# Kernel optimization log

Measured on AMD Instinct MI355X. Metric: run time of the kernel, lower is better.

The kernel has to match this reference:

```python
import jax, jax.numpy as jnp
import numpy as np

D_MODEL = 1024
NUM_HEADS = 16
HEAD_DIM = D_MODEL // NUM_HEADS


def setup_inputs() -> dict:
    key = jax.random.key(0)
    k_x, k_wqkv, k_bqkv, k_wo, k_bo = jax.random.split(key, 5)
    x = jax.random.normal(k_x, (2, 2048, D_MODEL), dtype=jnp.float32)
    s = 1.0 / np.sqrt(D_MODEL)
    W_qkv = jax.random.uniform(k_wqkv, (D_MODEL, 3 * D_MODEL), jnp.float32, -s, s)
    b_qkv = jax.random.uniform(k_bqkv, (3 * D_MODEL,), jnp.float32, -s, s)
    W_o = jax.random.uniform(k_wo, (D_MODEL, D_MODEL), jnp.float32, -s, s)
    b_o = jax.random.uniform(k_bo, (D_MODEL,), jnp.float32, -s, s)
    return {"x": x, "W_qkv": W_qkv, "b_qkv": b_qkv, "W_o": W_o, "b_o": b_o}


def reference(x, W_qkv, b_qkv, W_o, b_o):
    B, S, D = x.shape
    # fused QKV projection: [B,S,3D]
    qkv = jnp.einsum('bsd,de->bse', x, W_qkv) + b_qkv
    # [B,S,H,3*hd] -> [B,H,S,3*hd]
    qkv = qkv.reshape(B, S, NUM_HEADS, 3 * HEAD_DIM).transpose(0, 2, 1, 3)
    q, k, v = jnp.split(qkv, 3, axis=-1)  # each [B,H,S,hd]
    scale = 1.0 / jnp.sqrt(jnp.asarray(HEAD_DIM, dtype=x.dtype))
    scores = jnp.einsum('bhqd,bhkd->bhqk', q, k) * scale  # [B,H,S,S]
    attn = jax.nn.softmax(scores, axis=-1)
    values = jnp.einsum('bhqk,bhkd->bhqd', attn, v)  # [B,H,S,hd]
    values = values.transpose(0, 2, 1, 3).reshape(B, S, D)
    out = jnp.einsum('bsd,de->bse', values, W_o) + b_o
    return out
```

## Files before the change

### kernel.cpp

```cpp
#include <hip/hip_runtime.h>
#include <stdint.h>
#include <stddef.h>

typedef _Float16 f16;
typedef _Float16 f16x8 __attribute__((ext_vector_type(8)));
typedef _Float16 f16x4 __attribute__((ext_vector_type(4)));
typedef float    f32x2 __attribute__((ext_vector_type(2)));
typedef float    f32x4 __attribute__((ext_vector_type(4)));
typedef float    f32x16 __attribute__((ext_vector_type(16)));
typedef int      i32x4 __attribute__((ext_vector_type(4)));
typedef int      i32x2 __attribute__((ext_vector_type(2)));

#define S_LEN 2048
#define DM    1024
#define NH    16
#define HD    64
#define NTOK  4096
#define NQKV  3072
#define QSCALE 0.18033688011112042f

#if __has_builtin(__builtin_amdgcn_exp2f)
#define EXP2(x) __builtin_amdgcn_exp2f(x)
#else
#define EXP2(x) __expf((x) * 0.69314718055994531f)
#endif

__device__ __forceinline__ void gl_lds16(const void* g, void* l) {
  __builtin_amdgcn_global_load_lds(
      (const __attribute__((address_space(1))) void*)g,
      (__attribute__((address_space(3))) void*)l, 16, 0, 0);
}

__device__ __forceinline__ void pl32_swap(int& a, int& b) {
#if __has_builtin(__builtin_amdgcn_permlane32_swap)
  i32x2 r = __builtin_amdgcn_permlane32_swap(a, b, false, false);
  a = r.x; b = r.y;
#else
  asm volatile("v_permlane32_swap_b32 %0, %1" : "+v"(a), "+v"(b));
#endif
}

__device__ __forceinline__ float swap_half(float x, int hi) {
  int a = __builtin_bit_cast(int, x);
  int b = a;
  pl32_swap(a, b);
  return __builtin_bit_cast(float, hi ? a : b);
}

__device__ __forceinline__ int pkrtz(float a, float b) {
  auto h = __builtin_amdgcn_cvt_pkrtz(a, b);
  return __builtin_bit_cast(int, h);
}

__device__ __forceinline__ f16x8 mk_frag(int a, int b, int c, int d) {
  i32x4 v = {a, b, c, d};
  return __builtin_bit_cast(f16x8, v);
}

__device__ __forceinline__ f32x2 pk2(const f32x16& v, int i) {
  f32x2 r = {v[2*i], v[2*i+1]};
  return r;
}

__global__ __launch_bounds__(256) void cvt_f16_kernel(const float* __restrict__ in,
                                                      f16* __restrict__ out, int n) {
  int i = (blockIdx.x * 256 + threadIdx.x) * 8;
  if (i >= n) return;
  float4 a = *(const float4*)(in + i);
  float4 b = *(const float4*)(in + i + 4);
  f16x8 v = {(f16)a.x,(f16)a.y,(f16)a.z,(f16)a.w,(f16)b.x,(f16)b.y,(f16)b.z,(f16)b.w};
  *(f16x8*)(out + i) = v;
}

__global__ __launch_bounds__(256) void cvt_tr_kernel(const float* __restrict__ in,
                                                     f16* __restrict__ out, int R, int C) {
  __shared__ float t[32][33];
  int c0 = blockIdx.x * 32, r0 = blockIdx.y * 32;
  int tx = threadIdx.x, ty = threadIdx.y;
  #pragma unroll
  for (int i = 0; i < 4; ++i)
    t[ty + i*8][tx] = in[(size_t)(r0 + ty + i*8) * C + c0 + tx];
  __syncthreads();
  #pragma unroll
  for (int i = 0; i < 4; ++i)
    out[(size_t)(c0 + ty + i*8) * R + r0 + tx] = (f16)t[tx][ty + i*8];
}

template<int EPI>
__global__ __launch_bounds__(256) void gemm128_kernel(
    const f16* __restrict__ A, const f16* __restrict__ Bt,
    const float* __restrict__ bias,
    f16* __restrict__ qb, f16* __restrict__ kb, f16* __restrict__ vtb,
    float* __restrict__ out)
{
  __shared__ f16 As[128*32];
  __shared__ f16 Bs[128*32];
  const int tid = threadIdx.x;
  const int wid = tid >> 6, lane = tid & 63;
  const int g = lane >> 4, r = lane & 15;
  const int m0 = blockIdx.x * 128, n0 = blockIdx.y * 128;
  const int wm = (wid >> 1) * 64, wn = (wid & 1) * 64;

  f32x4 acc[4][4] = {};
  const int srow = tid >> 2;
  const int sch  = tid & 3;

  for (int kt = 0; kt < DM/32; ++kt) {
    const int k0 = kt * 32;
    __syncthreads();
    #pragma unroll
    for (int c = 0; c < 2; ++c) {
      int row = c*64 + srow;
      int sw = (sch ^ ((row >> 1) & 3)) * 8;
      gl_lds16(A  + (size_t)(m0 + row) * DM + k0 + sw, (char*)As + c*4096 + tid*16);
      gl_lds16(Bt + (size_t)(n0 + row) * DM + k0 + sw, (char*)Bs + c*4096 + tid*16);
    }
    __syncthreads();
    f16x8 a[4], b[4];
    #pragma unroll
    for (int mt = 0; mt < 4; ++mt) {
      int rl = wm + mt*16 + r;
      a[mt] = *(const f16x8*)(As + rl*32 + ((g ^ ((rl >> 1) & 3)) * 8));
    }
    #pragma unroll
    for (int nt = 0; nt < 4; ++nt) {
      int cl = wn + nt*16 + r;
      b[nt] = *(const f16x8*)(Bs + cl*32 + ((g ^ ((cl >> 1) & 3)) * 8));
    }
    #pragma unroll
    for (int mt = 0; mt < 4; ++mt)
      #pragma unroll
      for (int nt = 0; nt < 4; ++nt)
        acc[mt][nt] = __builtin_amdgcn_mfma_f32_16x16x32_f16(a[mt], b[nt], acc[mt][nt], 0, 0, 0);
  }

  if (EPI == 0) {
    #pragma unroll
    for (int mt = 0; mt < 4; ++mt) {
      int row0 = m0 + wm + mt*16 + g*4;
      int b_ = row0 >> 11, s0 = row0 & 2047;
      #pragma unroll
      for (int nt = 0; nt < 4; ++nt) {
        int col = n0 + wn + nt*16 + r;
        float bv = bias[col];
        int h = col / 192;
        int cc = col - h*192;
        int which = cc >> 6, d = cc & 63;
        size_t bh = (size_t)(b_*NH + h);
        if (which == 2) {
          f16x4 v;
          #pragma unroll
          for (int i = 0; i < 4; ++i) v[i] = (f16)(acc[mt][nt][i] + bv);
          *(f16x4*)(vtb + (bh*HD + d)*S_LEN + s0) = v;
        } else if (which == 0) {
          #pragma unroll
          for (int i = 0; i < 4; ++i)
            qb[(bh*S_LEN + s0 + i)*HD + d] = (f16)((acc[mt][nt][i] + bv) * QSCALE);
        } else {
          #pragma unroll
          for (int i = 0; i < 4; ++i)
            kb[(bh*S_LEN + s0 + i)*HD + d] = (f16)(acc[mt][nt][i] + bv);
        }
      }
    }
  } else {
    #pragma unroll
    for (int mt = 0; mt < 4; ++mt) {
      int row0 = m0 + wm + mt*16 + g*4;
      #pragma unroll
      for (int nt = 0; nt < 4; ++nt) {
        int col = n0 + wn + nt*16 + r;
        float bv = bias[col];
        #pragma unroll
        for (int i = 0; i < 4; ++i)
          out[(size_t)(row0 + i)*DM + col] = acc[mt][nt][i] + bv;
      }
    }
  }
}

__global__ __launch_bounds__(512, 4) void attn_kernel(
    const f16* __restrict__ qb, const f16* __restrict__ kb,
    const f16* __restrict__ vtb, f16* __restrict__ values)
{
  __shared__ __align__(16) char smem[66048];

  const int tid = threadIdx.x;
  const int wid = tid >> 6, lane = tid & 63;
  const int wq = wid & 3, wk = wid >> 2;
  const int ql = lane & 31, hi = lane >> 5;
  const int q0 = blockIdx.x * 128 + wq * 32;
  const int bh = blockIdx.y;
  const f16* qh = qb  + (size_t)bh * S_LEN * HD;
  const f16* kh = kb  + (size_t)bh * S_LEN * HD;
  const f16* vh = vtb + (size_t)bh * HD * S_LEN;
  const int kbase0 = wk * 1024;
  const int htid = tid & 255;

  int koff[2], voff[2];
  #pragma unroll
  for (int c = 0; c < 2; ++c) {
    int ca = htid + c*256, pr = ca >> 4, pc = ca & 15, lc = pc ^ (pr & 15);
    int row2 = pr*2 + (lc >> 3), e8 = (lc & 7) * 8;
    koff[c] = row2 * HD + e8;
    voff[c] = row2 * S_LEN + e8;
  }

  f16x8 qf[4];
  #pragma unroll
  for (int dk = 0; dk < 4; ++dk)
    qf[dk] = *(const f16x8*)(qh + (size_t)(q0 + ql)*HD + dk*16 + hi*8);

  const int r0b = (ql >> 1) << 8;
  const int xv  = (ql >> 1) & 15;
  const int hb  = ((ql & 1) << 3) | hi;

  f32x2 lacc = {0.f, 0.f};
  f32x16 o0 = {}, o1 = {};

  #define STAGE(kt_, buf_) do {                                            \
    const f16* ks_ = kh + (size_t)(kbase0 + (kt_)*64) * HD;                \
    const f16* vs_ = vh + (kbase0 + (kt_)*64);                             \
    char* kd_ = smem + (wk*2 + (buf_))*8192;                               \
    char* vd_ = smem + 32768 + (wk*2 + (buf_))*8192;                       \
    gl_lds16(ks_ + koff[0], kd_ + htid*16);                                \
    gl_lds16(ks_ + koff[1], kd_ + 4096 + htid*16);                         \
    gl_lds16(vs_ + voff[0], vd_ + htid*16);                                \
    gl_lds16(vs_ + voff[1], vd_ + 4096 + htid*16);                         \
  } while (0)

  STAGE(0, 0);
  __syncthreads();

  for (int kt = 0; kt < 16; ++kt) {
    const int cur = kt & 1;
    if (kt + 1 < 16) STAGE(kt + 1, cur ^ 1);

    const char* KsC = smem + (wk*2 + cur)*8192;
    const char* VsC = smem + 32768 + (wk*2 + cur)*8192;

    f32x16 s0 = {}, s1 = {};
    __builtin_amdgcn_s_setprio(1);
    #pragma unroll
    for (int dk = 0; dk < 4; ++dk) {
      int off = r0b + (((hb | (dk << 1)) ^ xv) << 4);
      f16x8 kf0 = *(const f16x8*)(KsC + off);
      f16x8 kf1 = *(const f16x8*)(KsC + 4096 + off);
      s0 = __builtin_amdgcn_mfma_f32_32x32x16_f16(kf0, qf[dk], s0, 0, 0, 0);
      s1 = __builtin_amdgcn_mfma_f32_32x32x16_f16(kf1, qf[dk], s1, 0, 0, 0);
    }
    __builtin_amdgcn_s_setprio(0);

    #pragma unroll
    for (int i = 0; i < 16; ++i) s0[i] = EXP2(s0[i]);
    #pragma unroll
    for (int i = 0; i < 16; ++i) s1[i] = EXP2(s1[i]);
    f32x2 sm[8];
    #pragma unroll
    for (int i = 0; i < 8; ++i) sm[i] = pk2(s0, i) + pk2(s1, i);
    #pragma unroll
    for (int i = 0; i < 4; ++i) sm[i] += sm[i+4];
    sm[0] += sm[1]; sm[2] += sm[3]; sm[0] += sm[2];
    lacc += sm[0];

    f16x8 pf[4];
    {
      int a = pkrtz(s0[0], s0[1]), b = pkrtz(s0[2], s0[3]);
      int c = pkrtz(s0[4], s0[5]), d = pkrtz(s0[6], s0[7]);
      pl32_swap(a, c); pl32_swap(b, d);
      pf[0] = mk_frag(a, b, c, d);
      a = pkrtz(s0[8],  s0[9]);  b = pkrtz(s0[10], s0[11]);
      c = pkrtz(s0[12], s0[13]); d = pkrtz(s0[14], s0[15]);
      pl32_swap(a, c); pl32_swap(b, d);
      pf[1] = mk_frag(a, b, c, d);
      a = pkrtz(s1[0], s1[1]); b = pkrtz(s1[2], s1[3]);
      c = pkrtz(s1[4], s1[5]); d = pkrtz(s1[6], s1[7]);
      pl32_swap(a, c); pl32_swap(b, d);
      pf[2] = mk_frag(a, b, c, d);
      a = pkrtz(s1[8],  s1[9]);  b = pkrtz(s1[10], s1[11]);
      c = pkrtz(s1[12], s1[13]); d = pkrtz(s1[14], s1[15]);
      pl32_swap(a, c); pl32_swap(b, d);
      pf[3] = mk_frag(a, b, c, d);
    }

    __builtin_amdgcn_s_setprio(1);
    #pragma unroll
    for (int w = 0; w < 4; ++w) {
      int off = r0b + (((hb | (w << 1)) ^ xv) << 4);
      f16x8 vf0 = *(const f16x8*)(VsC + off);
      f16x8 vf1 = *(const f16x8*)(VsC + 4096 + off);
      o0 = __builtin_amdgcn_mfma_f32_32x32x16_f16(pf[w], vf0, o0, 0, 0, 0);
      o1 = __builtin_amdgcn_mfma_f32_32x32x16_f16(pf[w], vf1, o1, 0, 0, 0);
    }
    __builtin_amdgcn_s_setprio(0);

    __syncthreads();
  }
  #undef STAGE

  float l_run = lacc.x + lacc.y;
  l_run += swap_half(l_run, hi);

  float* crow = ((float*)smem) + (wq*64 + lane)*36;
  float* cb   = (float*)(smem + 65536);
  if (wk == 1) {
    #pragma unroll
    for (int j = 0; j < 4; ++j) {
      f32x4 v0 = {o0[4*j], o0[4*j+1], o0[4*j+2], o0[4*j+3]};
      f32x4 v1 = {o1[4*j], o1[4*j+1], o1[4*j+2], o1[4*j+3]};
      *(f32x4*)(crow + j*4)      = v0;
      *(f32x4*)(crow + 16 + j*4) = v1;
    }
    crow[32] = l_run;
  }
  __syncthreads();
  if (wk == 0) {
    float inv = 1.0f / (l_run + crow[32]);
    cb[wq*32 + ql] = inv;
    f32x4 vinv[4], po0[4], po1[4];
    #pragma unroll
    for (int t = 0; t < 4; ++t) {
      vinv[t] = *(const f32x4*)&cb[wq*32 + hi*4 + t*8];
      po0[t]  = *(const f32x4*)(crow + t*4);
      po1[t]  = *(const f32x4*)(crow + 16 + t*4);
    }
    const int b_ = bh >> 4, h = bh & 15;
    #pragma unroll
    for (int t = 0; t < 4; ++t)
      #pragma unroll
      for (int i = 0; i < 4; ++i) {
        float v0 = (o0[t*4+i] + po0[t][i]) * vinv[t][i];
        float v1 = (o1[t*4+i] + po1[t][i]) * vinv[t][i];
        int qrow = q0 + 4*hi + 8*t + i;
        size_t base = (size_t)(b_*S_LEN + qrow) * DM + h*HD + ql;
        values[base]      = (f16)v0;
        values[base + 32] = (f16)v1;
      }
  }
}

extern "C" void kernel_launch(void* const* d_in, const int* in_sizes, int n_in,
                              void* d_out, int out_size, void* d_ws, size_t ws_size,
                              hipStream_t stream) {
  (void)in_sizes; (void)n_in; (void)out_size; (void)ws_size;
  const float* x    = (const float*)d_in[0];
  const float* Wqkv = (const float*)d_in[1];
  const float* bqkv = (const float*)d_in[2];
  const float* Wo   = (const float*)d_in[3];
  const float* bo   = (const float*)d_in[4];
  float* out = (float*)d_out;

  char* ws = (char*)d_ws;
  f16* x_h    = (f16*)(ws);
  f16* Wqkv_t = (f16*)(ws + ( 8ull<<20));
  f16* Wo_t   = (f16*)(ws + (14ull<<20));
  f16* qbuf   = (f16*)(ws + (16ull<<20));
  f16* kbuf   = (f16*)(ws + (24ull<<20));
  f16* vtbuf  = (f16*)(ws + (32ull<<20));
  f16* vals   = (f16*)(ws + (40ull<<20));

  cvt_f16_kernel<<<dim3(NTOK*DM/8/256), dim3(256), 0, stream>>>(x, x_h, NTOK*DM);
  cvt_tr_kernel<<<dim3(NQKV/32, DM/32), dim3(32, 8), 0, stream>>>(Wqkv, Wqkv_t, DM, NQKV);
  cvt_tr_kernel<<<dim3(DM/32, DM/32),  dim3(32, 8), 0, stream>>>(Wo, Wo_t, DM, DM);

  gemm128_kernel<0><<<dim3(NTOK/128, NQKV/128), dim3(256), 0, stream>>>(
      x_h, Wqkv_t, bqkv, qbuf, kbuf, vtbuf, nullptr);

  attn_kernel<<<dim3(S_LEN/128, 2*NH), dim3(512), 0, stream>>>(qbuf, kbuf, vtbuf, vals);

  gemm128_kernel<1><<<dim3(NTOK/128, DM/128), dim3(256), 0, stream>>>(
      vals, Wo_t, bo, nullptr, nullptr, nullptr, out);
}
```

Before: 120.3 us.

## Software-pipeline QK with softmax/PV in attention and remap blocks per XCD

The attention loop is restructured so the QK^T MFMAs for the next key tile are issued while the current tile's exp/pack and PV MFMAs run, with K and V staging split and prefetched separately. This is meant to overlap transcendental work with matrix-core work. In addition, all three main kernels switch to a flat 1-D grid whose index is remapped so blocks landing on the same XCD share rows/heads, improving L2 locality. Register pressure rises because s0/s1 stay live across iterations, which could hurt occupancy at 512x4 launch bounds.

```diff
diff --git a/kernel.cpp b/kernel.cpp
--- a/kernel.cpp
+++ b/kernel.cpp
@@ -98,7 +98,10 @@
   const int tid = threadIdx.x;
   const int wid = tid >> 6, lane = tid & 63;
   const int g = lane >> 4, r = lane & 15;
-  const int m0 = blockIdx.x * 128, n0 = blockIdx.y * 128;
+  const int flat = blockIdx.x;
+  const int xcd = flat & 7, idx = flat >> 3;
+  const int m0 = (xcd * 4 + (idx & 3)) * 128;
+  const int n0 = (idx >> 2) * 128;
   const int wm = (wid >> 1) * 64, wn = (wid & 1) * 64;
 
   f32x4 acc[4][4] = {};
@@ -189,8 +192,10 @@
   const int wid = tid >> 6, lane = tid & 63;
   const int wq = wid & 3, wk = wid >> 2;
   const int ql = lane & 31, hi = lane >> 5;
-  const int q0 = blockIdx.x * 128 + wq * 32;
-  const int bh = blockIdx.y;
+  const int flat = blockIdx.x;
+  const int xcd = flat & 7, idx = flat >> 3;
+  const int bh = xcd * 4 + (idx & 3);
+  const int q0 = (idx >> 2) * 128 + wq * 32;
   const f16* qh = qb  + (size_t)bh * S_LEN * HD;
   const f16* kh = kb  + (size_t)bh * S_LEN * HD;
   const f16* vh = vtb + (size_t)bh * HD * S_LEN;
@@ -217,86 +222,106 @@
 
   f32x2 lacc = {0.f, 0.f};
   f32x16 o0 = {}, o1 = {};
-
-  #define STAGE(kt_, buf_) do {                                            \
+  f32x16 s0, s1;
+
+  #define STAGE_K(kt_, buf_) do {                                          \
     const f16* ks_ = kh + (size_t)(kbase0 + (kt_)*64) * HD;                \
-    const f16* vs_ = vh + (kbase0 + (kt_)*64);                             \
     char* kd_ = smem + (wk*2 + (buf_))*8192;                               \
-    char* vd_ = smem + 32768 + (wk*2 + (buf_))*8192;                       \
     gl_lds16(ks_ + koff[0], kd_ + htid*16);                                \
     gl_lds16(ks_ + koff[1], kd_ + 4096 + htid*16);                         \
+  } while (0)
+  #define STAGE_V(kt_, buf_) do {                                          \
+    const f16* vs_ = vh + (kbase0 + (kt_)*64);                             \
+    char* vd_ = smem + 32768 + (wk*2 + (buf_))*8192;                       \
     gl_lds16(vs_ + voff[0], vd_ + htid*16);                                \
     gl_lds16(vs_ + voff[1], vd_ + 4096 + htid*16);                         \
   } while (0)
 
-  STAGE(0, 0);
-  __syncthreads();
-
-  for (int kt = 0; kt < 16; ++kt) {
+  #define QK(buf_) do {                                                    \
+    const char* KsC = smem + (wk*2 + (buf_))*8192;                         \
+    s0 = (f32x16){}; s1 = (f32x16){};                                      \
+    __builtin_amdgcn_s_setprio(1);                                         \
+    _Pragma("unroll")                                                      \
+    for (int dk = 0; dk < 4; ++dk) {                                       \
+      int off = r0b + (((hb | (dk << 1)) ^ xv) << 4);                      \
+      f16x8 kf0 = *(const f16x8*)(KsC + off);                              \
+      f16x8 kf1 = *(const f16x8*)(KsC + 4096 + off);                       \
+      s0 = __builtin_amdgcn_mfma_f32_32x32x16_f16(kf0, qf[dk], s0, 0, 0, 0);\
+      s1 = __builtin_amdgcn_mfma_f32_32x32x16_f16(kf1, qf[dk], s1, 0, 0, 0);\
+    }                                                                      \
+    __builtin_amdgcn_s_setprio(0);                                         \
+  } while (0)
+
+  #define EXP_PACK() do {                                                  \
+    _Pragma("unroll")                                                      \
+    for (int i = 0; i < 16; ++i) s0[i] = EXP2(s0[i]);                      \
+    _Pragma("unroll")                                                      \
+    for (int i = 0; i < 16; ++i) s1[i] = EXP2(s1[i]);                      \
+    f32x2 sm[8];                                                           \
+    _Pragma("unroll")                                                      \
+    for (int i = 0; i < 8; ++i) sm[i] = pk2(s0, i) + pk2(s1, i);           \
+    _Pragma("unroll")                                                      \
+    for (int i = 0; i < 4; ++i) sm[i] += sm[i+4];                          \
+    sm[0] += sm[1]; sm[2] += sm[3]; sm[0] += sm[2];                        \
+    lacc += sm[0];                                                         \
+    {                                                                      \
+      int a = pkrtz(s0[0], s0[1]), b = pkrtz(s0[2], s0[3]);                \
+      int c = pkrtz(s0[4], s0[5]), d = pkrtz(s0[6], s0[7]);                \
+      pl32_swap(a, c); pl32_swap(b, d);                                    \
+      pf[0] = mk_frag(a, b, c, d);                                         \
+      a = pkrtz(s0[8],  s0[9]);  b = pkrtz(s0[10], s0[11]);                \
+      c = pkrtz(s0[12], s0[13]); d = pkrtz(s0[14], s0[15]);                \
+      pl32_swap(a, c); pl32_swap(b, d);                                    \
+      pf[1] = mk_frag(a, b, c, d);                                         \
+      a = pkrtz(s1[0], s1[1]); b = pkrtz(s1[2], s1[3]);                    \
+      c = pkrtz(s1[4], s1[5]); d = pkrtz(s1[6], s1[7]);                    \
+      pl32_swap(a, c); pl32_swap(b, d);                                    \
+      pf[2] = mk_frag(a, b, c, d);                                         \
+      a = pkrtz(s1[8],  s1[9]);  b = pkrtz(s1[10], s1[11]);                \
+      c = pkrtz(s1[12], s1[13]); d = pkrtz(s1[14], s1[15]);                \
+      pl32_swap(a, c); pl32_swap(b, d);                                    \
+      pf[3] = mk_frag(a, b, c, d);                                         \
+    }                                                                      \
+  } while (0)
+
+  #define PV(buf_) do {                                                    \
+    const char* VsC = smem + 32768 + (wk*2 + (buf_))*8192;                 \
+    __builtin_amdgcn_s_setprio(1);                                         \
+    _Pragma("unroll")                                                      \
+    for (int w = 0; w < 4; ++w) {                                          \
+      int off = r0b + (((hb | (w << 1)) ^ xv) << 4);                       \
+      f16x8 vf0 = *(const f16x8*)(VsC + off);                              \
+      f16x8 vf1 = *(const f16x8*)(VsC + 4096 + off);                       \
+      o0 = __builtin_amdgcn_mfma_f32_32x32x16_f16(pf[w], vf0, o0, 0, 0, 0);\
+      o1 = __builtin_amdgcn_mfma_f32_32x32x16_f16(pf[w], vf1, o1, 0, 0, 0);\
+    }                                                                      \
+    __builtin_amdgcn_s_setprio(0);                                         \
+  } while (0)
+
+  STAGE_K(0, 0); STAGE_V(0, 0); STAGE_K(1, 1);
+  __syncthreads();
+  f16x8 pf[4];
+  QK(0);
+  __syncthreads();
+
+  for (int kt = 0; kt < 15; ++kt) {
     const int cur = kt & 1;
-    if (kt + 1 < 16) STAGE(kt + 1, cur ^ 1);
-
-    const char* KsC = smem + (wk*2 + cur)*8192;
-    const char* VsC = smem + 32768 + (wk*2 + cur)*8192;
-
-    f32x16 s0 = {}, s1 = {};
-    __builtin_amdgcn_s_setprio(1);
-    #pragma unroll
-    for (int dk = 0; dk < 4; ++dk) {
-      int off = r0b + (((hb | (dk << 1)) ^ xv) << 4);
-      f16x8 kf0 = *(const f16x8*)(KsC + off);
-      f16x8 kf1 = *(const f16x8*)(KsC + 4096 + off);
-      s0 = __builtin_amdgcn_mfma_f32_32x32x16_f16(kf0, qf[dk], s0, 0, 0, 0);
-      s1 = __builtin_amdgcn_mfma_f32_32x32x16_f16(kf1, qf[dk], s1, 0, 0, 0);
-    }
-    __builtin_amdgcn_s_setprio(0);
-
-    #pragma unroll
-    for (int i = 0; i < 16; ++i) s0[i] = EXP2(s0[i]);
-    #pragma unroll
-    for (int i = 0; i < 16; ++i) s1[i] = EXP2(s1[i]);
-    f32x2 sm[8];
-    #pragma unroll
-    for (int i = 0; i < 8; ++i) sm[i] = pk2(s0, i) + pk2(s1, i);
-    #pragma unroll
-    for (int i = 0; i < 4; ++i) sm[i] += sm[i+4];
-    sm[0] += sm[1]; sm[2] += sm[3]; sm[0] += sm[2];
-    lacc += sm[0];
-
-    f16x8 pf[4];
-    {
-      int a = pkrtz(s0[0], s0[1]), b = pkrtz(s0[2], s0[3]);
-      int c = pkrtz(s0[4], s0[5]), d = pkrtz(s0[6], s0[7]);
-      pl32_swap(a, c); pl32_swap(b, d);
-      pf[0] = mk_frag(a, b, c, d);
-      a = pkrtz(s0[8],  s0[9]);  b = pkrtz(s0[10], s0[11]);
-      c = pkrtz(s0[12], s0[13]); d = pkrtz(s0[14], s0[15]);
-      pl32_swap(a, c); pl32_swap(b, d);
-      pf[1] = mk_frag(a, b, c, d);
-      a = pkrtz(s1[0], s1[1]); b = pkrtz(s1[2], s1[3]);
-      c = pkrtz(s1[4], s1[5]); d = pkrtz(s1[6], s1[7]);
-      pl32_swap(a, c); pl32_swap(b, d);
-      pf[2] = mk_frag(a, b, c, d);
-      a = pkrtz(s1[8],  s1[9]);  b = pkrtz(s1[10], s1[11]);
-      c = pkrtz(s1[12], s1[13]); d = pkrtz(s1[14], s1[15]);
-      pl32_swap(a, c); pl32_swap(b, d);
-      pf[3] = mk_frag(a, b, c, d);
-    }
-
-    __builtin_amdgcn_s_setprio(1);
-    #pragma unroll
-    for (int w = 0; w < 4; ++w) {
-      int off = r0b + (((hb | (w << 1)) ^ xv) << 4);
-      f16x8 vf0 = *(const f16x8*)(VsC + off);
-      f16x8 vf1 = *(const f16x8*)(VsC + 4096 + off);
-      o0 = __builtin_amdgcn_mfma_f32_32x32x16_f16(pf[w], vf0, o0, 0, 0, 0);
-      o1 = __builtin_amdgcn_mfma_f32_32x32x16_f16(pf[w], vf1, o1, 0, 0, 0);
-    }
-    __builtin_amdgcn_s_setprio(0);
-
+    STAGE_V(kt + 1, cur ^ 1);
+    if (kt < 14) STAGE_K(kt + 2, cur);
+    EXP_PACK();
+    QK(cur ^ 1);
+    PV(cur);
     __syncthreads();
   }
-  #undef STAGE
+  EXP_PACK();
+  PV(1);
+  __syncthreads();
+
+  #undef STAGE_K
+  #undef STAGE_V
+  #undef QK
+  #undef EXP_PACK
+  #undef PV
 
   float l_run = lacc.x + lacc.y;
   l_run += swap_half(l_run, hi);
@@ -363,11 +388,11 @@
   cvt_tr_kernel<<<dim3(NQKV/32, DM/32), dim3(32, 8), 0, stream>>>(Wqkv, Wqkv_t, DM, NQKV);
   cvt_tr_kernel<<<dim3(DM/32, DM/32),  dim3(32, 8), 0, stream>>>(Wo, Wo_t, DM, DM);
 
-  gemm128_kernel<0><<<dim3(NTOK/128, NQKV/128), dim3(256), 0, stream>>>(
+  gemm128_kernel<0><<<dim3(768), dim3(256), 0, stream>>>(
       x_h, Wqkv_t, bqkv, qbuf, kbuf, vtbuf, nullptr);
 
-  attn_kernel<<<dim3(S_LEN/128, 2*NH), dim3(512), 0, stream>>>(qbuf, kbuf, vtbuf, vals);
-
-  gemm128_kernel<1><<<dim3(NTOK/128, DM/128), dim3(256), 0, stream>>>(
+  attn_kernel<<<dim3(512), dim3(512), 0, stream>>>(qbuf, kbuf, vtbuf, vals);
+
+  gemm128_kernel<1><<<dim3(256), dim3(256), 0, stream>>>(
       vals, Wo_t, bo, nullptr, nullptr, nullptr, out);
 }
```

New measurement: 118.6 us. No clear change (-1.4%).
